# Optimization experiments

Hardware: AMD Instinct MI355X
Metric: run time of the kernel (lower is better)

## Reference

```python
import jax, jax.numpy as jnp
import numpy as np

N = 100000
E = 1600000
D_IN = 128
HID = 128
N_CLASSES = 40
NEG_SLOPE = 0.2  # PyG GATConv default
BN_EPS = 1e-5


def setup_inputs() -> dict:
    key = jax.random.key(0)
    ks = jax.random.split(key, 16)
    s = 0.1
    return {
        "x": jax.random.normal(ks[0], (N, D_IN), dtype=jnp.float32),
        "edge_index": jax.random.randint(ks[1], (2, E), 0, N, dtype=jnp.int64),
        # GAT layer 1 (in=D_IN, out=HID, heads=1)
        "W1": jax.random.normal(ks[2], (D_IN, HID), dtype=jnp.float32) * s,
        "a_src1": jax.random.normal(ks[3], (HID,), dtype=jnp.float32) * s,
        "a_dst1": jax.random.normal(ks[4], (HID,), dtype=jnp.float32) * s,
        "b1": jnp.zeros((HID,), dtype=jnp.float32),
        # GAT layer 2 (in=HID, out=HID, heads=1)
        "W2": jax.random.normal(ks[5], (HID, HID), dtype=jnp.float32) * s,
        "a_src2": jax.random.normal(ks[6], (HID,), dtype=jnp.float32) * s,
        "a_dst2": jax.random.normal(ks[7], (HID,), dtype=jnp.float32) * s,
        "b2": jnp.zeros((HID,), dtype=jnp.float32),
        # shared BatchNorm1d(HID) applied after every conv
        "gamma": jnp.ones((HID,), dtype=jnp.float32),
        "beta": jnp.zeros((HID,), dtype=jnp.float32),
        # output Linear(HID, N_CLASSES)
        "Wout": jax.random.normal(ks[8], (HID, N_CLASSES), dtype=jnp.float32) * s,
        "bout": jnp.zeros((N_CLASSES,), dtype=jnp.float32),
    }


def reference(x, edge_index, W1, a_src1, a_dst1, b1, W2, a_src2, a_dst2, b2,
              gamma, beta, Wout, bout):
    n = x.shape[0]
    loops = jnp.arange(n, dtype=edge_index.dtype)  # add_self_loops (GATConv default)
    src = jnp.concatenate([edge_index[0], loops])
    dst = jnp.concatenate([edge_index[1], loops])

    def gat_layer(h_in, W, a_s, a_d, b):
        h = h_in @ W                                   # [N, HID]
        e_src = h @ a_s                                # [N] per-node src score
        e_dst = h @ a_d                                # [N] per-node dst score
        e = jax.nn.leaky_relu(e_src[src] + e_dst[dst], NEG_SLOPE)  # [E+N]
        # segment softmax over incoming edges of each dst node
        m = jax.ops.segment_max(e, dst, num_segments=n)
        p = jnp.exp(e - m[dst])
        denom = jax.ops.segment_sum(p, dst, num_segments=n)
        alpha = p / denom[dst]
        out = jax.ops.segment_sum(alpha[:, None] * h[src], dst, num_segments=n)
        return out + b

    def bn_elu(z):
        mu = z.mean(axis=0)
        var = ((z - mu) ** 2).mean(axis=0)  # biased var (BN training mode)
        zh = (z - mu) / jnp.sqrt(var + BN_EPS) * gamma + beta
        return jax.nn.elu(zh)

    h = bn_elu(gat_layer(x, W1, a_src1, a_dst1, b1))
    h = bn_elu(gat_layer(h, W2, a_src2, a_dst2, b2))
    return h @ Wout + bout
```

## Files before the change

### kernel.cpp

```cpp
#include <hip/hip_runtime.h>

#define NNODES 100000
#define NEDGES 1600000
#define ET (NEDGES + NNODES)
#define NBUCK 782
#define NEG 0.2f
#define BNEPS 1e-5f
#define EPB 4096
#define NBLK_E ((ET + EPB - 1) / EPB)

typedef __attribute__((ext_vector_type(8))) short short8;
typedef __attribute__((ext_vector_type(4))) float floatx4;
typedef __attribute__((ext_vector_type(2))) float floatx2;

__device__ __forceinline__ unsigned short f2b(float x) {
    unsigned int u = __float_as_uint(x);
    u += 0x7fff + ((u >> 16) & 1);
    return (unsigned short)(u >> 16);
}
__device__ __forceinline__ float b2f(unsigned short u) {
    return __uint_as_float(((unsigned int)u) << 16);
}
__device__ __forceinline__ float blo2f(unsigned int v) {
    return __uint_as_float(v << 16);
}
__device__ __forceinline__ float bhi2f(unsigned int v) {
    return __uint_as_float(v & 0xffff0000u);
}
__device__ __forceinline__ floatx2 u2f2(unsigned int v) {
    floatx2 r;
    r.x = __uint_as_float(v << 16);
    r.y = __uint_as_float(v & 0xffff0000u);
    return r;
}

__device__ __forceinline__ int edge_src(const int* ei, int e, int w64) {
    if (e >= NEDGES) return e - NEDGES;
    return w64 ? ei[2 * e] : ei[e];
}
__device__ __forceinline__ int edge_dst(const int* ei, int e, int w64) {
    if (e >= NEDGES) return e - NEDGES;
    return w64 ? ei[2 * (NEDGES + e)] : ei[NEDGES + e];
}

__global__ void k_prep(const float* __restrict__ W1, const float* __restrict__ W2,
                       unsigned short* __restrict__ WT1, unsigned short* __restrict__ WT2,
                       const int* ei, int* flag, int* bcnt, int* done, float* bnstat) {
    int t = blockIdx.x * 256 + threadIdx.x;
    if (t < 800) bcnt[t] = 0;
    if (blockIdx.x == 4) {
        bnstat[threadIdx.x] = 0.f;
    } else if (blockIdx.x == 5) {
        bnstat[256 + threadIdx.x] = 0.f;
    }
    if (t == 0) *done = 0;
    if (t == 1) {
        int is64 = 1;
        for (int j = 1; j < 16; j += 2)
            if (ei[j] != 0) is64 = 0;
        *flag = is64;
    }
    int k = t >> 7, n = t & 127;
    WT1[n * 128 + k] = f2b(W1[t]);
    WT2[n * 128 + k] = f2b(W2[t]);
}

__global__ __launch_bounds__(256) void k_bhist(const int* __restrict__ ei,
                                               const int* flag, int* bcnt,
                                               int* done, int* bbase, int* bcur) {
    __shared__ int lc[784];
    __shared__ int sh[256];
    __shared__ int lastf;
    int t = threadIdx.x;
    for (int i = t; i < NBUCK; i += 256) lc[i] = 0;
    __syncthreads();
    int w64 = *flag;
    int base = blockIdx.x * EPB;
    for (int j = 0; j < EPB / 512; j++) {
        int e = base + j * 512 + t * 2;
        if (e + 1 < NEDGES) {
            int d0, d1;
            if (w64) {
                int4 dv = *(const int4*)&ei[2 * (NEDGES + e)];
                d0 = dv.x; d1 = dv.z;
            } else {
                int2 dv = *(const int2*)&ei[NEDGES + e];
                d0 = dv.x; d1 = dv.y;
            }
            atomicAdd(&lc[d0 >> 7], 1);
            atomicAdd(&lc[d1 >> 7], 1);
        } else {
            for (int k = 0; k < 2; k++) {
                int ee = e + k;
                if (ee < ET) atomicAdd(&lc[edge_dst(ei, ee, w64) >> 7], 1);
            }
        }
    }
    __syncthreads();
    for (int i = t; i < NBUCK; i += 256)
        if (lc[i]) atomicAdd(&bcnt[i], lc[i]);
    __threadfence();
    __syncthreads();
    if (t == 0) lastf = (atomicAdd(done, 1) == gridDim.x - 1) ? 1 : 0;
    __syncthreads();
    if (!lastf) return;
    int vals[4], pre[4], sum = 0;
#pragma unroll
    for (int i = 0; i < 4; i++) {
        int id = t * 4 + i;
        int v = (id < NBUCK) ? atomicAdd(&bcnt[id], 0) : 0;
        pre[i] = sum; vals[i] = v; sum += v;
    }
    sh[t] = sum;
    __syncthreads();
    for (int off = 1; off < 256; off <<= 1) {
        int add = (t >= off) ? sh[t - off] : 0;
        __syncthreads();
        sh[t] += add;
        __syncthreads();
    }
    int excl = sh[t] - sum;
#pragma unroll
    for (int i = 0; i < 4; i++) {
        int id = t * 4 + i;
        if (id < NBUCK) { bbase[id] = excl + pre[i]; bcur[id] = excl + pre[i]; }
    }
    if (t == 255) bbase[NBUCK] = sh[255];
    (void)vals;
}

__global__ __launch_bounds__(256) void k_bscatter(const int* __restrict__ ei,
                                                  const int* flag, int* bcur,
                                                  int* __restrict__ pairs) {
    __shared__ int lc[784];
    __shared__ int lbase[784];
    int t = threadIdx.x;
    for (int i = t; i < NBUCK; i += 256) lc[i] = 0;
    __syncthreads();
    int w64 = *flag;
    int base = blockIdx.x * EPB;
    for (int j = 0; j < EPB / 512; j++) {
        int e = base + j * 512 + t * 2;
        if (e + 1 < NEDGES) {
            int d0, d1;
            if (w64) {
                int4 dv = *(const int4*)&ei[2 * (NEDGES + e)];
                d0 = dv.x; d1 = dv.z;
            } else {
                int2 dv = *(const int2*)&ei[NEDGES + e];
                d0 = dv.x; d1 = dv.y;
            }
            atomicAdd(&lc[d0 >> 7], 1);
            atomicAdd(&lc[d1 >> 7], 1);
        } else {
            for (int k = 0; k < 2; k++) {
                int ee = e + k;
                if (ee < ET) atomicAdd(&lc[edge_dst(ei, ee, w64) >> 7], 1);
            }
        }
    }
    __syncthreads();
    for (int i = t; i < NBUCK; i += 256)
        if (lc[i]) lbase[i] = atomicAdd(&bcur[i], lc[i]);
    __syncthreads();
    for (int j = 0; j < EPB / 512; j++) {
        int e = base + j * 512 + t * 2;
        if (e + 1 < NEDGES) {
            int s0, s1, d0, d1;
            if (w64) {
                int4 sv = *(const int4*)&ei[2 * e];
                int4 dv = *(const int4*)&ei[2 * (NEDGES + e)];
                s0 = sv.x; s1 = sv.z; d0 = dv.x; d1 = dv.z;
            } else {
                int2 sv = *(const int2*)&ei[e];
                int2 dv = *(const int2*)&ei[NEDGES + e];
                s0 = sv.x; s1 = sv.y; d0 = dv.x; d1 = dv.y;
            }
            int p0 = atomicAdd(&lbase[d0 >> 7], 1);
            pairs[p0] = (s0 << 7) | (d0 & 127);
            int p1 = atomicAdd(&lbase[d1 >> 7], 1);
            pairs[p1] = (s1 << 7) | (d1 & 127);
        } else {
            for (int k = 0; k < 2; k++) {
                int ee = e + k;
                if (ee < ET) {
                    int src = edge_src(ei, ee, w64);
                    int dst = edge_dst(ei, ee, w64);
                    int pos = atomicAdd(&lbase[dst >> 7], 1);
                    pairs[pos] = (src << 7) | (dst & 127);
                }
            }
        }
    }
}

__global__ __launch_bounds__(256) void k_bsort(const int* __restrict__ pairs,
                                               const int* __restrict__ bbase,
                                               int* __restrict__ rowptr,
                                               int* __restrict__ srcs) {
    __shared__ int ncnt[128];
    __shared__ int nbase[128];
    __shared__ int sscan[128];
    int b = blockIdx.x, t = threadIdx.x;
    if (t < 128) ncnt[t] = 0;
    __syncthreads();
    int s0 = bbase[b], s1 = bbase[b + 1];
    for (int i = s0 + t; i < s1; i += 256)
        atomicAdd(&ncnt[pairs[i] & 127], 1);
    __syncthreads();
    int v = (t < 128) ? ncnt[t] : 0;
    if (t < 128) sscan[t] = v;
    __syncthreads();
    for (int off = 1; off < 128; off <<= 1) {
        int add = (t < 128 && t >= off) ? sscan[t - off] : 0;
        __syncthreads();
        if (t < 128) sscan[t] += add;
        __syncthreads();
    }
    if (t < 128) {
        int excl = sscan[t] - v;
        nbase[t] = excl;
        int node = b * 128 + t;
        if (node <= NNODES) rowptr[node] = s0 + excl;
    }
    __syncthreads();
    if (t < 128) ncnt[t] = nbase[t];
    __syncthreads();
    for (int i = s0 + t; i < s1; i += 256) {
        int pr = pairs[i];
        int off = atomicAdd(&ncnt[pr & 127], 1);
        srcs[s0 + off] = ((unsigned int)pr) >> 7;
    }
}

template<bool BN>
__global__ __launch_bounds__(256) void k_gemm(const void* __restrict__ Ain,
        const unsigned short* __restrict__ WTg,
        const float* __restrict__ sums, const float* __restrict__ sqs,
        const float* __restrict__ gamma, const float* __restrict__ beta,
        const float* __restrict__ a_s, const float* __restrict__ a_d,
        float* __restrict__ es, float* __restrict__ ed,
        unsigned short* __restrict__ hB, int n) {
    __shared__ unsigned short lA[128][136];
    __shared__ unsigned short lW[128][136];
    __shared__ float las[128], lad[128];
    __shared__ float lsc[128], lsh[128];
    int t = threadIdx.x;
    int row0 = blockIdx.x * 128;
    if (t < 128) { las[t] = a_s[t]; lad[t] = a_d[t]; }
    if (BN && t < 128) {
        float mu = sums[t] * (1.f / NNODES);
        float var = fmaxf(sqs[t] * (1.f / NNODES) - mu * mu, 0.f);
        float s = gamma[t] * rsqrtf(var + BNEPS);
        lsc[t] = s;
        lsh[t] = beta[t] - mu * s;
    }

    const uint4* wt4 = (const uint4*)WTg;
#pragma unroll
    for (int j = 0; j < 8; j++) {
        int idx = t + j * 256;
        *(uint4*)&lW[idx >> 4][(idx & 15) * 8] = wt4[idx];
    }
    if (BN) __syncthreads();

    if (BN) {
        const uint4* Ab = (const uint4*)Ain;
#pragma unroll
        for (int j = 0; j < 8; j++) {
            int idx = t + j * 256;
            int r = idx >> 4, seg = idx & 15;
            uint4 v = make_uint4(0, 0, 0, 0);
            if (row0 + r < n) v = Ab[(size_t)(row0 + r) * 16 + seg];
            float f[8];
            f[0] = blo2f(v.x); f[1] = bhi2f(v.x);
            f[2] = blo2f(v.y); f[3] = bhi2f(v.y);
            f[4] = blo2f(v.z); f[5] = bhi2f(v.z);
            f[6] = blo2f(v.w); f[7] = bhi2f(v.w);
            unsigned short us[8];
#pragma unroll
            for (int k = 0; k < 8; k++) {
                int c = seg * 8 + k;
                float z = fmaf(f[k], lsc[c], lsh[c]);
                z = z > 0.f ? z : __expf(z) - 1.f;
                us[k] = f2b(z);
            }
            ushort4 u0, u1;
            u0.x = us[0]; u0.y = us[1]; u0.z = us[2]; u0.w = us[3];
            u1.x = us[4]; u1.y = us[5]; u1.z = us[6]; u1.w = us[7];
            *(ushort4*)&lA[r][seg * 8] = u0;
            *(ushort4*)&lA[r][seg * 8 + 4] = u1;
        }
    } else {
        const float* Af = (const float*)Ain;
#pragma unroll
        for (int j = 0; j < 16; j++) {
            int idx = t + j * 256;
            int r = idx >> 5, c4 = idx & 31;
            float4 v = make_float4(0.f, 0.f, 0.f, 0.f);
            if (row0 + r < n) v = ((const float4*)Af)[(size_t)(row0 + r) * 32 + c4];
            ushort4 u;
            u.x = f2b(v.x); u.y = f2b(v.y); u.z = f2b(v.z); u.w = f2b(v.w);
            *(ushort4*)&lA[r][c4 * 4] = u;
        }
    }
    __syncthreads();

    int w = t >> 6, lane = t & 63;
    int m = lane & 15, q = lane >> 4;
    int ar0 = w * 32 + m, ar1 = w * 32 + 16 + m;
    floatx4 acc0[8], acc1[8];
#pragma unroll
    for (int ct = 0; ct < 8; ct++) { acc0[ct] = (floatx4)0.0f; acc1[ct] = (floatx4)0.0f; }

#pragma unroll
    for (int kt = 0; kt < 4; kt++) {
        int kb = kt * 32 + q * 8;
        short8 af0 = *(const short8*)&lA[ar0][kb];
        short8 af1 = *(const short8*)&lA[ar1][kb];
#pragma unroll
        for (int ct = 0; ct < 8; ct++) {
            short8 bf = *(const short8*)&lW[ct * 16 + m][kb];
            acc0[ct] = __builtin_amdgcn_mfma_f32_16x16x32_bf16(af0, bf, acc0[ct], 0, 0, 0);
            acc1[ct] = __builtin_amdgcn_mfma_f32_16x16x32_bf16(af1, bf, acc1[ct], 0, 0, 0);
        }
    }

    __syncthreads();
#pragma unroll
    for (int ct = 0; ct < 8; ct++)
#pragma unroll
        for (int r = 0; r < 4; r++) {
            lA[w * 32 + q * 4 + r][ct * 16 + m] = f2b(acc0[ct][r]);
            lA[w * 32 + 16 + q * 4 + r][ct * 16 + m] = f2b(acc1[ct][r]);
        }
    __syncthreads();
#pragma unroll
    for (int j = 0; j < 8; j++) {
        int idx = t + j * 256;
        int r = idx >> 4, seg = idx & 15;
        int grow = row0 + r;
        if (grow < n) {
            uint4 v = *(const uint4*)&lA[r][seg * 8];
            ((uint4*)hB)[(size_t)grow * 16 + seg] = v;
        }
    }
    int r = t >> 1, q2 = t & 1;
    float s1 = 0.f, s2 = 0.f;
#pragma unroll
    for (int k = 0; k < 32; k++) {
        int c = q2 * 64 + 2 * k;
        unsigned int u = *(const unsigned int*)&lA[r][c];
        float va = blo2f(u), vb = bhi2f(u);
        s1 += va * las[c] + vb * las[c + 1];
        s2 += va * lad[c] + vb * lad[c + 1];
    }
    s1 += __shfl_xor(s1, 1, 64);
    s2 += __shfl_xor(s2, 1, 64);
    if (q2 == 0 && row0 + r < n) { es[row0 + r] = s1; ed[row0 + r] = s2; }
}

__global__ __launch_bounds__(256) void k_attn(const unsigned short* __restrict__ hB,
                                              const int* __restrict__ srcs,
                                              const int* __restrict__ rowptr,
                                              const float* __restrict__ es,
                                              const float* __restrict__ ed,
                                              const float* __restrict__ bias,
                                              unsigned short* __restrict__ haggB, int n) {
    __shared__ uint2 sp[8][32];
    int w = (blockIdx.x * 256 + threadIdx.x) >> 5;
    if (w >= n) return;
    int hw = threadIdx.x >> 5;
    int lane32 = threadIdx.x & 31;
    int g = lane32 >> 4, l16 = lane32 & 15;
    int start = rowptr[w], end = rowptr[w + 1];
    float edv = ed[w];
    const uint4* hp4 = (const uint4*)hB;
    floatx2 a0 = {0.f, 0.f}, a1 = {0.f, 0.f}, a2 = {0.f, 0.f}, a3 = {0.f, 0.f};
    float den = 0.f;

    for (int chunk = start; chunk < end; chunk += 32) {
        int i = chunk + lane32;
        int sv = 0; float pv = 0.f;
        if (i < end) {
            sv = srcs[i];
            float e = es[sv] + edv;
            e = e > 0.f ? e : NEG * e;
            pv = __expf(e);
            den += pv;
        }
        sp[hw][lane32] = make_uint2((unsigned)sv, __float_as_uint(pv));
        int cnt = min(32, end - chunk);
        for (int j = 0; j < cnt; j += 8) {
            uint2 e0 = sp[hw][j + g];
            uint2 e1 = sp[hw][j + 2 + g];
            uint2 e2 = sp[hw][j + 4 + g];
            uint2 e3 = sp[hw][j + 6 + g];
            uint4 h0 = hp4[e0.x * 16u + l16];
            uint4 h1 = hp4[e1.x * 16u + l16];
            uint4 h2 = hp4[e2.x * 16u + l16];
            uint4 h3 = hp4[e3.x * 16u + l16];
            float p0 = __uint_as_float(e0.y), p1 = __uint_as_float(e1.y);
            float p2 = __uint_as_float(e2.y), p3 = __uint_as_float(e3.y);
            floatx2 P0 = {p0, p0};
            a0 += P0 * u2f2(h0.x); a1 += P0 * u2f2(h0.y);
            a2 += P0 * u2f2(h0.z); a3 += P0 * u2f2(h0.w);
            floatx2 P1 = {p1, p1};
            a0 += P1 * u2f2(h1.x); a1 += P1 * u2f2(h1.y);
            a2 += P1 * u2f2(h1.z); a3 += P1 * u2f2(h1.w);
            floatx2 P2 = {p2, p2};
            a0 += P2 * u2f2(h2.x); a1 += P2 * u2f2(h2.y);
            a2 += P2 * u2f2(h2.z); a3 += P2 * u2f2(h2.w);
            floatx2 P3 = {p3, p3};
            a0 += P3 * u2f2(h3.x); a1 += P3 * u2f2(h3.y);
            a2 += P3 * u2f2(h3.z); a3 += P3 * u2f2(h3.w);
        }
    }
    den += __shfl_xor(den, 1, 64);  den += __shfl_xor(den, 2, 64);
    den += __shfl_xor(den, 4, 64);  den += __shfl_xor(den, 8, 64);
    den += __shfl_xor(den, 16, 64);
    a0.x += __shfl_xor(a0.x, 16, 64); a0.y += __shfl_xor(a0.y, 16, 64);
    a1.x += __shfl_xor(a1.x, 16, 64); a1.y += __shfl_xor(a1.y, 16, 64);
    a2.x += __shfl_xor(a2.x, 16, 64); a2.y += __shfl_xor(a2.y, 16, 64);
    a3.x += __shfl_xor(a3.x, 16, 64); a3.y += __shfl_xor(a3.y, 16, 64);
    if (g == 0) {
        float inv = 1.f / den;
        const float2* b2p = (const float2*)bias;
        float2 c0 = b2p[l16 * 4 + 0], c1 = b2p[l16 * 4 + 1];
        float2 c2 = b2p[l16 * 4 + 2], c3 = b2p[l16 * 4 + 3];
        uint4 o;
        o.x = (unsigned int)f2b(fmaf(a0.x, inv, c0.x)) |
              ((unsigned int)f2b(fmaf(a0.y, inv, c0.y)) << 16);
        o.y = (unsigned int)f2b(fmaf(a1.x, inv, c1.x)) |
              ((unsigned int)f2b(fmaf(a1.y, inv, c1.y)) << 16);
        o.z = (unsigned int)f2b(fmaf(a2.x, inv, c2.x)) |
              ((unsigned int)f2b(fmaf(a2.y, inv, c2.y)) << 16);
        o.w = (unsigned int)f2b(fmaf(a3.x, inv, c3.x)) |
              ((unsigned int)f2b(fmaf(a3.y, inv, c3.y)) << 16);
        ((uint4*)haggB)[(size_t)w * 16 + l16] = o;
    }
}

__global__ __launch_bounds__(256) void k_bnstats(const unsigned short* __restrict__ hin,
                                                 float* sums, float* sqs, int n) {
    __shared__ float red[4][256];
    int t = threadIdx.x;
    int c2 = t & 63, quarter = t >> 6;
    int r0 = blockIdx.x * 256;
    int rend = min(r0 + 256, n);
    const unsigned int* hp = (const unsigned int*)hin;
    float s0 = 0.f, q0 = 0.f, s1 = 0.f, q1 = 0.f;
    for (int r = r0 + quarter; r < rend; r += 4) {
        unsigned int v = hp[(size_t)r * 64 + c2];
        float a = blo2f(v), b = bhi2f(v);
        s0 += a; q0 += a * a;
        s1 += b; q1 += b * b;
    }
    *(float4*)&red[quarter][c2 * 4] = make_float4(s0, q0, s1, q1);
    __syncthreads();
    float v = red[0][t] + red[1][t] + red[2][t] + red[3][t];
    int c2i = t >> 2, k = t & 3;
    int ch = c2i * 2 + (k >> 1);
    if (k & 1) atomicAdd(&sqs[ch], v);
    else       atomicAdd(&sums[ch], v);
}

__global__ __launch_bounds__(256) void k_outgemm(const unsigned short* __restrict__ h,
                                                 const float* __restrict__ sums,
                                                 const float* __restrict__ sqs,
                                                 const float* __restrict__ gamma,
                                                 const float* __restrict__ beta,
                                                 const float* __restrict__ Wout,
                                                 const float* __restrict__ bout,
                                                 float* __restrict__ out, int n) {
    __shared__ float lw[128 * 40];
    __shared__ float lsc[128], lsh[128];
    int t = threadIdx.x;
    if (t < 128) {
        float mu = sums[t] * (1.f / NNODES);
        float var = fmaxf(sqs[t] * (1.f / NNODES) - mu * mu, 0.f);
        float s = gamma[t] * rsqrtf(var + BNEPS);
        lsc[t] = s;
        lsh[t] = beta[t] - mu * s;
    }
    for (int i = t; i < 128 * 40; i += 256) lw[i] = Wout[i];
    __syncthreads();
    int idx = blockIdx.x * 256 + t;
    int row = idx >> 1, jq = idx & 1;
    if (row >= n) return;
    const uint4* hb4 = (const uint4*)h;
    float acc[40];
#pragma unroll
    for (int j = 0; j < 40; j++) acc[j] = 0.f;
#pragma unroll
    for (int s8 = 0; s8 < 8; s8++) {
        int seg = jq * 8 + s8;
        uint4 v = hb4[(size_t)row * 16 + seg];
        float f[8];
        f[0] = blo2f(v.x); f[1] = bhi2f(v.x);
        f[2] = blo2f(v.y); f[3] = bhi2f(v.y);
        f[4] = blo2f(v.z); f[5] = bhi2f(v.z);
        f[6] = blo2f(v.w); f[7] = bhi2f(v.w);
#pragma unroll
        for (int k = 0; k < 8; k++) {
            int c = seg * 8 + k;
            float z = fmaf(f[k], lsc[c], lsh[c]);
            z = z > 0.f ? z : __expf(z) - 1.f;
            const float4* wr = (const float4*)&lw[c * 40];
#pragma unroll
            for (int j4 = 0; j4 < 10; j4++) {
                float4 wv = wr[j4];
                acc[j4 * 4 + 0] = fmaf(z, wv.x, acc[j4 * 4 + 0]);
                acc[j4 * 4 + 1] = fmaf(z, wv.y, acc[j4 * 4 + 1]);
                acc[j4 * 4 + 2] = fmaf(z, wv.z, acc[j4 * 4 + 2]);
                acc[j4 * 4 + 3] = fmaf(z, wv.w, acc[j4 * 4 + 3]);
            }
        }
    }
#pragma unroll
    for (int j = 0; j < 40; j++) acc[j] += __shfl_xor(acc[j], 1, 64);
    if (jq == 0) {
        const float4* b4 = (const float4*)bout;
        float4* outp = (float4*)(out + (size_t)row * 40);
#pragma unroll
        for (int j4 = 0; j4 < 10; j4++) {
            float4 bv = b4[j4];
            float4 o;
            o.x = acc[j4 * 4 + 0] + bv.x;
            o.y = acc[j4 * 4 + 1] + bv.y;
            o.z = acc[j4 * 4 + 2] + bv.z;
            o.w = acc[j4 * 4 + 3] + bv.w;
            outp[j4] = o;
        }
    }
}

extern "C" void kernel_launch(void* const* d_in, const int* in_sizes, int n_in,
                              void* d_out, int out_size, void* d_ws, size_t ws_size,
                              hipStream_t stream) {
    const float* x      = (const float*)d_in[0];
    const int*   ei     = (const int*)d_in[1];
    const float* W1     = (const float*)d_in[2];
    const float* a_src1 = (const float*)d_in[3];
    const float* a_dst1 = (const float*)d_in[4];
    const float* b1     = (const float*)d_in[5];
    const float* W2     = (const float*)d_in[6];
    const float* a_src2 = (const float*)d_in[7];
    const float* a_dst2 = (const float*)d_in[8];
    const float* b2     = (const float*)d_in[9];
    const float* gamma  = (const float*)d_in[10];
    const float* beta   = (const float*)d_in[11];
    const float* Wout   = (const float*)d_in[12];
    const float* bout   = (const float*)d_in[13];
    float* out = (float*)d_out;

    char* p = (char*)d_ws;
    auto alloc = [&](size_t bytes) -> void* {
        void* r = (void*)p;
        p += (bytes + 255) & ~(size_t)255;
        return r;
    };
    unsigned short* hB    = (unsigned short*)alloc((size_t)NNODES * 128 * 2);
    unsigned short* haggB = (unsigned short*)alloc((size_t)NNODES * 128 * 2);
    float* es     = (float*)alloc((size_t)NNODES * 4);
    float* ed     = (float*)alloc((size_t)NNODES * 4);
    int*   pairs  = (int*)alloc((size_t)ET * 4);
    int*   srcs   = (int*)alloc((size_t)ET * 4);
    int*   rowptr = (int*)alloc((size_t)(NNODES + 1) * 4);
    int*   bcnt   = (int*)alloc(800 * 4);
    int*   bbase  = (int*)alloc(800 * 4);
    int*   bcur   = (int*)alloc(800 * 4);
    float* bnstat = (float*)alloc(4 * 128 * 4);
    unsigned short* WT1 = (unsigned short*)alloc(128 * 128 * 2);
    unsigned short* WT2 = (unsigned short*)alloc(128 * 128 * 2);
    int*   flag   = (int*)alloc(4);
    int*   done   = (int*)alloc(4);

    float* sum1 = bnstat, *sq1 = bnstat + 128, *sum2 = bnstat + 256, *sq2 = bnstat + 384;

    k_prep<<<64, 256, 0, stream>>>(W1, W2, WT1, WT2, ei, flag, bcnt, done, bnstat);
    k_bhist<<<NBLK_E, 256, 0, stream>>>(ei, flag, bcnt, done, bbase, bcur);
    k_bscatter<<<NBLK_E, 256, 0, stream>>>(ei, flag, bcur, pairs);
    k_bsort<<<NBUCK, 256, 0, stream>>>(pairs, bbase, rowptr, srcs);

    const int GB = (NNODES + 127) / 128;
    const int AB = NNODES / 8;
    const int SB = (NNODES + 255) / 256;
    const int OB = (NNODES * 2 + 255) / 256;

    k_gemm<false><<<GB, 256, 0, stream>>>(x, WT1, nullptr, nullptr, nullptr, nullptr,
                                          a_src1, a_dst1, es, ed, hB, NNODES);
    k_attn<<<AB, 256, 0, stream>>>(hB, srcs, rowptr, es, ed, b1, haggB, NNODES);
    k_bnstats<<<SB, 256, 0, stream>>>(haggB, sum1, sq1, NNODES);

    k_gemm<true><<<GB, 256, 0, stream>>>(haggB, WT2, sum1, sq1, gamma, beta,
                                         a_src2, a_dst2, es, ed, hB, NNODES);
    k_attn<<<AB, 256, 0, stream>>>(hB, srcs, rowptr, es, ed, b2, haggB, NNODES);
    k_bnstats<<<SB, 256, 0, stream>>>(haggB, sum2, sq2, NNODES);

    k_outgemm<<<OB, 256, 0, stream>>>(haggB, sum2, sq2, gamma, beta, Wout, bout, out, NNODES);

    (void)in_sizes; (void)n_in; (void)out_size; (void)ws_size;
}
```

Before: 447.4 us.

## Split output GEMM K-halves across waves and read wave-uniform weights from global

The output linear kernel now assigns each K-half of a row to a different wavefront instead of to adjacent lanes. Within a wave every lane reads the same weight address, so weights come straight from global memory as uniform (scalar-friendly) loads and are no longer staged in LDS. The two partial sums are combined through a padded LDS buffer rather than a lane shuffle, and all hidden-row loads are issued up front into registers. The cost is an extra barrier and LDS traffic for the reduction, plus higher register pressure from the prefetched row data.

```diff
diff --git a/kernel.cpp b/kernel.cpp
--- a/kernel.cpp
+++ b/kernel.cpp
@@ -473,8 +473,8 @@
                                                  const float* __restrict__ Wout,
                                                  const float* __restrict__ bout,
                                                  float* __restrict__ out, int n) {
-    __shared__ float lw[128 * 40];
     __shared__ float lsc[128], lsh[128];
+    __shared__ float lacc[2][64][41];
     int t = threadIdx.x;
     if (t < 128) {
         float mu = sums[t] * (1.f / NNODES);
@@ -483,53 +483,63 @@
         lsc[t] = s;
         lsh[t] = beta[t] - mu * s;
     }
-    for (int i = t; i < 128 * 40; i += 256) lw[i] = Wout[i];
-    __syncthreads();
-    int idx = blockIdx.x * 256 + t;
-    int row = idx >> 1, jq = idx & 1;
-    if (row >= n) return;
+    __syncthreads();
+    int wv = __builtin_amdgcn_readfirstlane(t >> 6);
+    int lane = t & 63;
+    int pairId = wv >> 1, jq = wv & 1;
+    int row = blockIdx.x * 128 + pairId * 64 + lane;
+    bool valid = row < n;
     const uint4* hb4 = (const uint4*)h;
+    uint4 hreg[8];
+#pragma unroll
+    for (int s8 = 0; s8 < 8; s8++) {
+        hreg[s8] = make_uint4(0, 0, 0, 0);
+        if (valid) hreg[s8] = hb4[(size_t)row * 16 + jq * 8 + s8];
+    }
+    const float* wbase = Wout + jq * 64 * 40;
     float acc[40];
 #pragma unroll
     for (int j = 0; j < 40; j++) acc[j] = 0.f;
 #pragma unroll
-    for (int s8 = 0; s8 < 8; s8++) {
-        int seg = jq * 8 + s8;
-        uint4 v = hb4[(size_t)row * 16 + seg];
+    for (int k8 = 0; k8 < 8; k8++) {
+        uint4 v = hreg[k8];
         float f[8];
         f[0] = blo2f(v.x); f[1] = bhi2f(v.x);
         f[2] = blo2f(v.y); f[3] = bhi2f(v.y);
         f[4] = blo2f(v.z); f[5] = bhi2f(v.z);
         f[6] = blo2f(v.w); f[7] = bhi2f(v.w);
 #pragma unroll
-        for (int k = 0; k < 8; k++) {
-            int c = seg * 8 + k;
-            float z = fmaf(f[k], lsc[c], lsh[c]);
+        for (int kk = 0; kk < 8; kk++) {
+            int c = jq * 64 + k8 * 8 + kk;
+            float z = fmaf(f[kk], lsc[c], lsh[c]);
             z = z > 0.f ? z : __expf(z) - 1.f;
-            const float4* wr = (const float4*)&lw[c * 40];
+            const float4* wr = (const float4*)(wbase + (k8 * 8 + kk) * 40);
 #pragma unroll
             for (int j4 = 0; j4 < 10; j4++) {
-                float4 wv = wr[j4];
-                acc[j4 * 4 + 0] = fmaf(z, wv.x, acc[j4 * 4 + 0]);
-                acc[j4 * 4 + 1] = fmaf(z, wv.y, acc[j4 * 4 + 1]);
-                acc[j4 * 4 + 2] = fmaf(z, wv.z, acc[j4 * 4 + 2]);
-                acc[j4 * 4 + 3] = fmaf(z, wv.w, acc[j4 * 4 + 3]);
-            }
-        }
-    }
-#pragma unroll
-    for (int j = 0; j < 40; j++) acc[j] += __shfl_xor(acc[j], 1, 64);
-    if (jq == 0) {
+                float4 wv4 = wr[j4];
+                acc[j4 * 4 + 0] = fmaf(z, wv4.x, acc[j4 * 4 + 0]);
+                acc[j4 * 4 + 1] = fmaf(z, wv4.y, acc[j4 * 4 + 1]);
+                acc[j4 * 4 + 2] = fmaf(z, wv4.z, acc[j4 * 4 + 2]);
+                acc[j4 * 4 + 3] = fmaf(z, wv4.w, acc[j4 * 4 + 3]);
+            }
+        }
+    }
+    if (jq == 1) {
+#pragma unroll
+        for (int j = 0; j < 40; j++) lacc[pairId][lane][j] = acc[j];
+    }
+    __syncthreads();
+    if (jq == 0 && valid) {
         const float4* b4 = (const float4*)bout;
         float4* outp = (float4*)(out + (size_t)row * 40);
 #pragma unroll
         for (int j4 = 0; j4 < 10; j4++) {
             float4 bv = b4[j4];
             float4 o;
-            o.x = acc[j4 * 4 + 0] + bv.x;
-            o.y = acc[j4 * 4 + 1] + bv.y;
-            o.z = acc[j4 * 4 + 2] + bv.z;
-            o.w = acc[j4 * 4 + 3] + bv.w;
+            o.x = acc[j4 * 4 + 0] + lacc[pairId][lane][j4 * 4 + 0] + bv.x;
+            o.y = acc[j4 * 4 + 1] + lacc[pairId][lane][j4 * 4 + 1] + bv.y;
+            o.z = acc[j4 * 4 + 2] + lacc[pairId][lane][j4 * 4 + 2] + bv.z;
+            o.w = acc[j4 * 4 + 3] + lacc[pairId][lane][j4 * 4 + 3] + bv.w;
             outp[j4] = o;
         }
     }
@@ -586,7 +596,7 @@
     const int GB = (NNODES + 127) / 128;
     const int AB = NNODES / 8;
     const int SB = (NNODES + 255) / 256;
-    const int OB = (NNODES * 2 + 255) / 256;
+    const int OB = (NNODES + 127) / 128;
 
     k_gemm<false><<<GB, 256, 0, stream>>>(x, WT1, nullptr, nullptr, nullptr, nullptr,
                                           a_src1, a_dst1, es, ed, hB, NNODES);
```

New measurement: 437.2 us. -2.3%, faster.
